# Kernel optimization log

Measured on AMD Instinct MI355X. Metric: run time of the kernel, lower is better.

## Reference

```python
import jax, jax.numpy as jnp
import numpy as np

D_MODEL = 512
N_HEADS = 8
D_FF = 2048

def _linear_params(key, d_in, d_out):
    kw, kb = jax.random.split(key)
    bound = 1.0 / np.sqrt(d_in)
    W = jax.random.uniform(kw, (d_in, d_out), minval=-bound, maxval=bound, dtype=jnp.float32)
    b = jax.random.uniform(kb, (d_out,), minval=-bound, maxval=bound, dtype=jnp.float32)
    return W, b

def setup_inputs() -> dict:
    key = jax.random.key(0)
    ks = jax.random.split(key, 7)
    x = jax.random.normal(ks[0], (4, 2048, D_MODEL), dtype=jnp.float32)
    Wq, bq = _linear_params(ks[1], D_MODEL, D_MODEL)
    Wk, bk = _linear_params(ks[2], D_MODEL, D_MODEL)
    Wv, bv = _linear_params(ks[3], D_MODEL, D_MODEL)
    W1, b1 = _linear_params(ks[4], D_MODEL, D_FF)
    W2, b2 = _linear_params(ks[5], D_FF, D_MODEL)
    g1 = jnp.ones((D_MODEL,), jnp.float32); be1 = jnp.zeros((D_MODEL,), jnp.float32)
    g2 = jnp.ones((D_MODEL,), jnp.float32); be2 = jnp.zeros((D_MODEL,), jnp.float32)
    return {"x": x, "Wq": Wq, "bq": bq, "Wk": Wk, "bk": bk, "Wv": Wv, "bv": bv,
            "W1": W1, "b1": b1, "W2": W2, "b2": b2,
            "g1": g1, "be1": be1, "g2": g2, "be2": be2}

def _layernorm(x, g, b, eps=1e-5):
    mu = jnp.mean(x, axis=-1, keepdims=True)
    var = jnp.mean(jnp.square(x - mu), axis=-1, keepdims=True)
    return (x - mu) * jax.lax.rsqrt(var + eps) * g + b

def reference(x, Wq, bq, Wk, bk, Wv, bv, W1, b1, W2, b2, g1, be1, g2, be2):
    B, S, D = x.shape
    H = N_HEADS
    Dh = D // H
    residual = x
    xn = _layernorm(x, g1, be1)
    # [B,S,D] -> [B,H,S,Dh]
    q = (xn @ Wq + bq).reshape(B, S, H, Dh).transpose(0, 2, 1, 3)
    k = (xn @ Wk + bk).reshape(B, S, H, Dh).transpose(0, 2, 1, 3)
    v = (xn @ Wv + bv).reshape(B, S, H, Dh).transpose(0, 2, 1, 3)
    # sigmoid pointwise attention, scaled by sqrt(d_model) (not head dim)
    scores = jnp.einsum('bhsd,bhtd->bhst', q, k) / jnp.sqrt(jnp.float32(D))
    attn = jax.nn.sigmoid(scores)
    out = jnp.einsum('bhst,bhtd->bhsd', attn, v)
    out = out.transpose(0, 2, 1, 3).reshape(B, S, D)
    x = residual + out  # dropout=0 (eval)
    residual = x
    xn = _layernorm(x, g2, be2)
    ffn = jax.nn.relu(xn @ W1 + b1) @ W2 + b2
    return residual + ffn
```

## Files before the change

kernel.cpp:

```cpp
#include <hip/hip_runtime.h>
#include <hip/hip_bf16.h>
#include <math.h>

#define D_MODEL 512
#define N_HEADS 8
#define D_HEAD 64
#define D_FF 2048
#define SEQ 2048
#define BATCH 4
#define NTOK (BATCH * SEQ)
#define QSCALE 0.04419417382415922f

typedef unsigned short ushort_t;
typedef __attribute__((ext_vector_type(8))) short short8;
typedef __attribute__((ext_vector_type(4))) float float4v;

static __device__ __forceinline__ ushort_t f2bf(float f) {
    union { float f; unsigned int i; } c; c.f = f;
    unsigned int i = c.i;
    unsigned int r = (i + 0x7FFFu + ((i >> 16) & 1u)) >> 16;
    return (ushort_t)r;
}

static __device__ __forceinline__ unsigned int pack2bf(float a, float b) {
    union { __hip_bfloat162 h; unsigned int u; } c;
    c.h = __float22bfloat162_rn(make_float2(a, b));
    return c.u;
}

static __device__ __forceinline__ float sigmoid_f(float x) {
    return __builtin_amdgcn_rcpf(1.0f + __expf(-x));
}

__global__ __launch_bounds__(256) void k_transpose_w(const float* __restrict__ W,
                                                     ushort_t* __restrict__ Wt,
                                                     int K, int N) {
    int id = blockIdx.x * 256 + threadIdx.x;
    if (id >= K * N) return;
    int k = id / N, n = id - k * N;
    Wt[(size_t)n * K + k] = f2bf(W[id]);
}

__global__ __launch_bounds__(256) void k_layernorm(const float* __restrict__ X,
                                                   const float* __restrict__ g,
                                                   const float* __restrict__ be,
                                                   ushort_t* __restrict__ Out) {
    int row  = blockIdx.x * 4 + (threadIdx.x >> 6);
    int lane = threadIdx.x & 63;
    const float* x = X + (size_t)row * D_MODEL + lane * 8;
    float4 v0 = ((const float4*)x)[0];
    float4 v1 = ((const float4*)x)[1];
    float vals[8] = {v0.x, v0.y, v0.z, v0.w, v1.x, v1.y, v1.z, v1.w};
    float s = 0.f, sq = 0.f;
#pragma unroll
    for (int j = 0; j < 8; j++) { s += vals[j]; sq += vals[j] * vals[j]; }
#pragma unroll
    for (int off = 32; off; off >>= 1) { s += __shfl_xor(s, off); sq += __shfl_xor(sq, off); }
    float mu  = s * (1.0f / D_MODEL);
    float var = sq * (1.0f / D_MODEL) - mu * mu;
    float inv = rsqrtf(var + 1e-5f);
    const float* gp  = g  + lane * 8;
    const float* bp  = be + lane * 8;
    float4 g0 = ((const float4*)gp)[0], g1v = ((const float4*)gp)[1];
    float4 b0 = ((const float4*)bp)[0], b1v = ((const float4*)bp)[1];
    float gs[8] = {g0.x, g0.y, g0.z, g0.w, g1v.x, g1v.y, g1v.z, g1v.w};
    float bs[8] = {b0.x, b0.y, b0.z, b0.w, b1v.x, b1v.y, b1v.z, b1v.w};
    ushort_t o[8];
#pragma unroll
    for (int j = 0; j < 8; j++) o[j] = f2bf((vals[j] - mu) * inv * gs[j] + bs[j]);
    ushort_t* op = Out + (size_t)row * D_MODEL + lane * 8;
    *(uint4*)op = *(uint4*)o;
}

__device__ __forceinline__ void gemm_core(const ushort_t* __restrict__ A,
                                          const ushort_t* __restrict__ Bt,
                                          int K, int m0, int n0,
                                          ushort_t (*As)[128][40], ushort_t (*Bs)[128][40],
                                          float4v acc[4][4]) {
    int t = threadIdx.x, w = t >> 6, l = t & 63, q = l >> 4, lm = l & 15;
    int mb = (w & 1) * 64, nb = (w >> 1) * 64;
    int srow = t >> 1, scol = (t & 1) * 16;
    const ushort_t* ag0 = A  + (size_t)(m0 + srow) * K + scol;
    const ushort_t* bg0 = Bt + (size_t)(n0 + srow) * K + scol;

    uint4 ar0 = *(const uint4*)(ag0),     ar1 = *(const uint4*)(ag0 + 8);
    uint4 br0 = *(const uint4*)(bg0),     br1 = *(const uint4*)(bg0 + 8);
    *(uint4*)&As[0][srow][scol] = ar0; *(uint4*)&As[0][srow][scol + 8] = ar1;
    *(uint4*)&Bs[0][srow][scol] = br0; *(uint4*)&Bs[0][srow][scol + 8] = br1;
    int T = K >> 5;
    ar0 = *(const uint4*)(ag0 + 32); ar1 = *(const uint4*)(ag0 + 40);
    br0 = *(const uint4*)(bg0 + 32); br1 = *(const uint4*)(bg0 + 40);
    __syncthreads();

    for (int kt = 0; kt < T; kt++) {
        int cur = kt & 1;
        short8 a[4], b[4];
#pragma unroll
        for (int i = 0; i < 4; i++) a[i] = *(const short8*)&As[cur][mb + 16 * i + lm][q * 8];
#pragma unroll
        for (int j = 0; j < 4; j++) b[j] = *(const short8*)&Bs[cur][nb + 16 * j + lm][q * 8];
#pragma unroll
        for (int i = 0; i < 4; i++)
#pragma unroll
            for (int j = 0; j < 4; j++)
                acc[i][j] = __builtin_amdgcn_mfma_f32_16x16x32_bf16(a[i], b[j], acc[i][j], 0, 0, 0);
        if (kt + 1 < T) {
            int nxt = 1 - cur;
            *(uint4*)&As[nxt][srow][scol] = ar0; *(uint4*)&As[nxt][srow][scol + 8] = ar1;
            *(uint4*)&Bs[nxt][srow][scol] = br0; *(uint4*)&Bs[nxt][srow][scol + 8] = br1;
            if (kt + 2 < T) {
                const ushort_t* ag = ag0 + (kt + 2) * 32;
                const ushort_t* bg = bg0 + (kt + 2) * 32;
                ar0 = *(const uint4*)(ag); ar1 = *(const uint4*)(ag + 8);
                br0 = *(const uint4*)(bg); br1 = *(const uint4*)(bg + 8);
            }
        }
        __syncthreads();
    }
}

__global__ __launch_bounds__(256) void k_gemm_qkv(const ushort_t* __restrict__ A,
                                                  const ushort_t* __restrict__ Bt,
                                                  const float* __restrict__ bq,
                                                  const float* __restrict__ bk,
                                                  const float* __restrict__ bv,
                                                  ushort_t* __restrict__ qb,
                                                  ushort_t* __restrict__ kb,
                                                  ushort_t* __restrict__ vt) {
    __shared__ ushort_t As[2][128][40];
    __shared__ ushort_t Bs[2][128][40];
    int m0 = blockIdx.x * 128, n0 = blockIdx.y * 128;
    float4v acc[4][4];
#pragma unroll
    for (int i = 0; i < 4; i++)
#pragma unroll
        for (int j = 0; j < 4; j++) acc[i][j] = (float4v){0.f, 0.f, 0.f, 0.f};
    gemm_core(A, Bt, D_MODEL, m0, n0, As, Bs, acc);

    int t = threadIdx.x, w = t >> 6, l = t & 63, q = l >> 4, lm = l & 15;
    int mb = (w & 1) * 64, nb = (w >> 1) * 64;
    int mat = n0 >> 9, c0 = n0 & 511;
    const float* bias = (mat == 0) ? bq : ((mat == 1) ? bk : bv);
#pragma unroll
    for (int j = 0; j < 4; j++) {
        int cl = c0 + nb + 16 * j + lm;
        int hh = cl >> 6, dh = cl & 63;
        float bvv = bias[cl];
#pragma unroll
        for (int i = 0; i < 4; i++) {
            int mr0 = m0 + mb + 16 * i + q * 4;
            int bb = mr0 >> 11, ss0 = mr0 & (SEQ - 1);
            if (mat == 2) {
                union { ushort_t s[4]; uint2 v; } pk;
#pragma unroll
                for (int r = 0; r < 4; r++) pk.s[r] = f2bf(acc[i][j][r] + bvv);
                *(uint2*)&vt[((size_t)(bb * N_HEADS + hh) * D_HEAD + dh) * SEQ + ss0] = pk.v;
            } else {
                ushort_t* dst = (mat == 0) ? qb : kb;
                float sc = (mat == 0) ? QSCALE : 1.0f;
#pragma unroll
                for (int r = 0; r < 4; r++)
                    dst[((size_t)(bb * N_HEADS + hh) * SEQ + ss0 + r) * D_HEAD + dh] =
                        f2bf((acc[i][j][r] + bvv) * sc);
            }
        }
    }
}

__global__ __launch_bounds__(256) void k_gemm_ffn1(const ushort_t* __restrict__ A,
                                                   const ushort_t* __restrict__ Bt,
                                                   const float* __restrict__ b1,
                                                   ushort_t* __restrict__ hb) {
    __shared__ ushort_t As[2][128][40];
    __shared__ ushort_t Bs[2][128][40];
    int m0 = blockIdx.x * 128, n0 = blockIdx.y * 128;
    float4v acc[4][4];
#pragma unroll
    for (int i = 0; i < 4; i++)
#pragma unroll
        for (int j = 0; j < 4; j++) acc[i][j] = (float4v){0.f, 0.f, 0.f, 0.f};
    gemm_core(A, Bt, D_MODEL, m0, n0, As, Bs, acc);

    int t = threadIdx.x, w = t >> 6, l = t & 63, q = l >> 4, lm = l & 15;
    int mb = (w & 1) * 64, nb = (w >> 1) * 64;
#pragma unroll
    for (int j = 0; j < 4; j++) {
        int cl = n0 + nb + 16 * j + lm;
        float bvv = b1[cl];
#pragma unroll
        for (int i = 0; i < 4; i++) {
            int mr0 = m0 + mb + 16 * i + q * 4;
#pragma unroll
            for (int r = 0; r < 4; r++)
                hb[(size_t)(mr0 + r) * D_FF + cl] = f2bf(fmaxf(acc[i][j][r] + bvv, 0.f));
        }
    }
}

__global__ __launch_bounds__(256) void k_gemm_ffn2(const ushort_t* __restrict__ A,
                                                   const ushort_t* __restrict__ Bt,
                                                   const float* __restrict__ b2,
                                                   const float* __restrict__ res,
                                                   float* __restrict__ out) {
    __shared__ ushort_t As[2][128][40];
    __shared__ ushort_t Bs[2][128][40];
    int m0 = blockIdx.x * 128, n0 = blockIdx.y * 128;
    float4v acc[4][4];
#pragma unroll
    for (int i = 0; i < 4; i++)
#pragma unroll
        for (int j = 0; j < 4; j++) acc[i][j] = (float4v){0.f, 0.f, 0.f, 0.f};
    gemm_core(A, Bt, D_FF, m0, n0, As, Bs, acc);

    int t = threadIdx.x, w = t >> 6, l = t & 63, q = l >> 4, lm = l & 15;
    int mb = (w & 1) * 64, nb = (w >> 1) * 64;
#pragma unroll
    for (int j = 0; j < 4; j++) {
        int cl = n0 + nb + 16 * j + lm;
        float bvv = b2[cl];
#pragma unroll
        for (int i = 0; i < 4; i++) {
            int mr0 = m0 + mb + 16 * i + q * 4;
#pragma unroll
            for (int r = 0; r < 4; r++) {
                size_t idx = (size_t)(mr0 + r) * D_MODEL + cl;
                out[idx] = acc[i][j][r] + bvv + res[idx];
            }
        }
    }
}

__global__ __launch_bounds__(256) void k_attention(const ushort_t* __restrict__ Q,
                                                   const ushort_t* __restrict__ Kb,
                                                   const ushort_t* __restrict__ Vt,
                                                   const float* __restrict__ X,
                                                   float* __restrict__ Y) {
    __shared__ ushort_t Ks[2][64][72];
    __shared__ ushort_t Vs[2][64][72];
    __shared__ ushort_t Ps[128][72];
    int bh = blockIdx.y;
    int b = bh >> 3, h = bh & 7;
    size_t base = (size_t)bh * SEQ * D_HEAD;
    int s0 = blockIdx.x * 128;
    int t = threadIdx.x, w = t >> 6, l = t & 63, q = l >> 4, lm = l & 15;
    int srow = t >> 2, sc = (t & 3) * 16;

    short8 qf[2][2];
#pragma unroll
    for (int nt = 0; nt < 2; nt++)
#pragma unroll
        for (int kc = 0; kc < 2; kc++) {
            const ushort_t* qg = Q + base + (size_t)(s0 + 32 * w + 16 * nt + lm) * D_HEAD + kc * 32 + q * 8;
            uint4 u = *(const uint4*)qg;
            qf[nt][kc] = *(const short8*)&u;
        }

    float4v o[2][4];
#pragma unroll
    for (int nt = 0; nt < 2; nt++)
#pragma unroll
        for (int dj = 0; dj < 4; dj++) o[nt][dj] = (float4v){0.f, 0.f, 0.f, 0.f};

    uint4 kr0, kr1, vr0, vr1;
    const ushort_t* kg0 = Kb + base + (size_t)srow * D_HEAD + sc;
    const ushort_t* vg0 = Vt + base + (size_t)srow * SEQ + sc;

    kr0 = *(const uint4*)(kg0); kr1 = *(const uint4*)(kg0 + 8);
    vr0 = *(const uint4*)(vg0); vr1 = *(const uint4*)(vg0 + 8);
    *(uint4*)&Ks[0][srow][sc] = kr0; *(uint4*)&Ks[0][srow][sc + 8] = kr1;
    *(uint4*)&Vs[0][srow][sc] = vr0; *(uint4*)&Vs[0][srow][sc + 8] = vr1;
    kr0 = *(const uint4*)(kg0 + 64 * D_HEAD); kr1 = *(const uint4*)(kg0 + 64 * D_HEAD + 8);
    vr0 = *(const uint4*)(vg0 + 64);          vr1 = *(const uint4*)(vg0 + 64 + 8);
    __syncthreads();

    for (int tt = 0; tt < SEQ / 64; tt++) {
        int cur = tt & 1;
        float4v st[4][2];
#pragma unroll
        for (int mt = 0; mt < 4; mt++)
#pragma unroll
            for (int nt = 0; nt < 2; nt++) st[mt][nt] = (float4v){0.f, 0.f, 0.f, 0.f};
#pragma unroll
        for (int kc = 0; kc < 2; kc++) {
            short8 a[4];
#pragma unroll
            for (int mt = 0; mt < 4; mt++) a[mt] = *(const short8*)&Ks[cur][16 * mt + lm][kc * 32 + q * 8];
#pragma unroll
            for (int mt = 0; mt < 4; mt++)
#pragma unroll
                for (int nt = 0; nt < 2; nt++)
                    st[mt][nt] = __builtin_amdgcn_mfma_f32_16x16x32_bf16(a[mt], qf[nt][kc], st[mt][nt], 0, 0, 0);
        }
#pragma unroll
        for (int mt = 0; mt < 4; mt++)
#pragma unroll
            for (int nt = 0; nt < 2; nt++) {
                float4v s4 = st[mt][nt];
                uint2 pk;
                pk.x = pack2bf(sigmoid_f(s4[0]), sigmoid_f(s4[1]));
                pk.y = pack2bf(sigmoid_f(s4[2]), sigmoid_f(s4[3]));
                *(uint2*)&Ps[32 * w + 16 * nt + lm][16 * mt + 4 * q] = pk;
            }
#pragma unroll
        for (int kc = 0; kc < 2; kc++) {
            short8 ap[2], bv[4];
#pragma unroll
            for (int nt = 0; nt < 2; nt++) ap[nt] = *(const short8*)&Ps[32 * w + 16 * nt + lm][kc * 32 + q * 8];
#pragma unroll
            for (int dj = 0; dj < 4; dj++) bv[dj] = *(const short8*)&Vs[cur][16 * dj + lm][kc * 32 + q * 8];
#pragma unroll
            for (int nt = 0; nt < 2; nt++)
#pragma unroll
                for (int dj = 0; dj < 4; dj++)
                    o[nt][dj] = __builtin_amdgcn_mfma_f32_16x16x32_bf16(ap[nt], bv[dj], o[nt][dj], 0, 0, 0);
        }
        if (tt + 1 < SEQ / 64) {
            int nxt = 1 - cur;
            *(uint4*)&Ks[nxt][srow][sc] = kr0; *(uint4*)&Ks[nxt][srow][sc + 8] = kr1;
            *(uint4*)&Vs[nxt][srow][sc] = vr0; *(uint4*)&Vs[nxt][srow][sc + 8] = vr1;
            if (tt + 2 < SEQ / 64) {
                const ushort_t* kg = kg0 + (size_t)(tt + 2) * 64 * D_HEAD;
                const ushort_t* vg = vg0 + (tt + 2) * 64;
                kr0 = *(const uint4*)(kg); kr1 = *(const uint4*)(kg + 8);
                vr0 = *(const uint4*)(vg); vr1 = *(const uint4*)(vg + 8);
            }
        }
        __syncthreads();
    }

#pragma unroll
    for (int nt = 0; nt < 2; nt++)
#pragma unroll
        for (int dj = 0; dj < 4; dj++) {
            int d = 16 * dj + lm;
#pragma unroll
            for (int r = 0; r < 4; r++) {
                int s = s0 + 32 * w + 16 * nt + q * 4 + r;
                size_t idx = ((size_t)(b * SEQ + s)) * D_MODEL + h * D_HEAD + d;
                Y[idx] = X[idx] + o[nt][dj][r];
            }
        }
}

extern "C" void kernel_launch(void* const* d_in, const int* in_sizes, int n_in,
                              void* d_out, int out_size, void* d_ws, size_t ws_size,
                              hipStream_t stream) {
    const float* x   = (const float*)d_in[0];
    const float* Wq  = (const float*)d_in[1];
    const float* bq  = (const float*)d_in[2];
    const float* Wk  = (const float*)d_in[3];
    const float* bk  = (const float*)d_in[4];
    const float* Wv  = (const float*)d_in[5];
    const float* bv  = (const float*)d_in[6];
    const float* W1  = (const float*)d_in[7];
    const float* b1  = (const float*)d_in[8];
    const float* W2  = (const float*)d_in[9];
    const float* b2  = (const float*)d_in[10];
    const float* g1  = (const float*)d_in[11];
    const float* be1 = (const float*)d_in[12];
    const float* g2  = (const float*)d_in[13];
    const float* be2 = (const float*)d_in[14];
    float* out = (float*)d_out;

    char* p = (char*)d_ws;
    ushort_t* xn    = (ushort_t*)p; p += (size_t)NTOK * D_MODEL * 2;
    ushort_t* yn    = (ushort_t*)p; p += (size_t)NTOK * D_MODEL * 2;
    float*    y     = (float*)p;    p += (size_t)NTOK * D_MODEL * 4;
    ushort_t* qb    = (ushort_t*)p; p += (size_t)NTOK * D_MODEL * 2;
    ushort_t* kb    = (ushort_t*)p; p += (size_t)NTOK * D_MODEL * 2;
    ushort_t* vt    = (ushort_t*)p; p += (size_t)NTOK * D_MODEL * 2;
    ushort_t* hb    = (ushort_t*)p; p += (size_t)NTOK * D_FF * 2;
    ushort_t* Wqkvt = (ushort_t*)p; p += (size_t)3 * D_MODEL * D_MODEL * 2;
    ushort_t* W1t   = (ushort_t*)p; p += (size_t)D_MODEL * D_FF * 2;
    ushort_t* W2t   = (ushort_t*)p; p += (size_t)D_FF * D_MODEL * 2;

    k_transpose_w<<<(D_MODEL * D_MODEL + 255) / 256, 256, 0, stream>>>(Wq, Wqkvt, D_MODEL, D_MODEL);
    k_transpose_w<<<(D_MODEL * D_MODEL + 255) / 256, 256, 0, stream>>>(Wk, Wqkvt + (size_t)D_MODEL * D_MODEL, D_MODEL, D_MODEL);
    k_transpose_w<<<(D_MODEL * D_MODEL + 255) / 256, 256, 0, stream>>>(Wv, Wqkvt + (size_t)2 * D_MODEL * D_MODEL, D_MODEL, D_MODEL);
    k_transpose_w<<<(D_MODEL * D_FF + 255) / 256, 256, 0, stream>>>(W1, W1t, D_MODEL, D_FF);
    k_transpose_w<<<(D_FF * D_MODEL + 255) / 256, 256, 0, stream>>>(W2, W2t, D_FF, D_MODEL);

    k_layernorm<<<NTOK / 4, 256, 0, stream>>>(x, g1, be1, xn);

    dim3 gq(NTOK / 128, (3 * D_MODEL) / 128);
    k_gemm_qkv<<<gq, 256, 0, stream>>>(xn, Wqkvt, bq, bk, bv, qb, kb, vt);

    dim3 ga(SEQ / 128, BATCH * N_HEADS);
    k_attention<<<ga, 256, 0, stream>>>(qb, kb, vt, x, y);

    k_layernorm<<<NTOK / 4, 256, 0, stream>>>(y, g2, be2, yn);

    dim3 g1d(NTOK / 128, D_FF / 128);
    k_gemm_ffn1<<<g1d, 256, 0, stream>>>(yn, W1t, b1, hb);
    dim3 g2d(NTOK / 128, D_MODEL / 128);
    k_gemm_ffn2<<<g2d, 256, 0, stream>>>(hb, W2t, b2, y, out);
}
```

Before: 275.0 us.

## Keep attention probabilities in registers, merge weight-prep kernels, vectorize output

The attention kernel now feeds the sigmoid probabilities straight from the score MFMA accumulators into a 16x16x16 bf16 MFMA as register operands. This removes the shared-memory P buffer and its write/read round trip, and computes the transposed output with V as the A operand. The five weight-transpose launches are merged into one kernel to cut launch overhead. The attention epilogue now does float4 residual loads and stores instead of scalar ones. The trade-off is using the smaller-K MFMA instruction, which means more MFMA issues for the same work.

Result: no change. 274.8 us (-0.1%).

```diff
diff --git a/kernel.cpp b/kernel.cpp
--- a/kernel.cpp
+++ b/kernel.cpp
@@ -13,6 +13,7 @@
 
 typedef unsigned short ushort_t;
 typedef __attribute__((ext_vector_type(8))) short short8;
+typedef __attribute__((ext_vector_type(4))) short short4v;
 typedef __attribute__((ext_vector_type(4))) float float4v;
 
 static __device__ __forceinline__ ushort_t f2bf(float f) {
@@ -32,13 +33,33 @@
     return __builtin_amdgcn_rcpf(1.0f + __expf(-x));
 }
 
-__global__ __launch_bounds__(256) void k_transpose_w(const float* __restrict__ W,
-                                                     ushort_t* __restrict__ Wt,
-                                                     int K, int N) {
+__global__ __launch_bounds__(256) void k_prep_weights(const float* __restrict__ Wq,
+                                                      const float* __restrict__ Wk,
+                                                      const float* __restrict__ Wv,
+                                                      const float* __restrict__ W1,
+                                                      const float* __restrict__ W2,
+                                                      ushort_t* __restrict__ Wqkvt,
+                                                      ushort_t* __restrict__ W1t,
+                                                      ushort_t* __restrict__ W2t) {
     int id = blockIdx.x * 256 + threadIdx.x;
-    if (id >= K * N) return;
-    int k = id / N, n = id - k * N;
-    Wt[(size_t)n * K + k] = f2bf(W[id]);
+    if (id < 3 * 262144) {
+        int m = id >> 18, r = id & 262143;
+        int k = r >> 9, n = r & 511;
+        const float* src = (m == 0) ? Wq : ((m == 1) ? Wk : Wv);
+        Wqkvt[((size_t)m * 512 + n) * 512 + k] = f2bf(src[r]);
+        return;
+    }
+    int id2 = id - 3 * 262144;
+    if (id2 < 1048576) {
+        int k = id2 >> 11, n = id2 & 2047;
+        W1t[(size_t)n * 512 + k] = f2bf(W1[id2]);
+        return;
+    }
+    int id3 = id2 - 1048576;
+    if (id3 < 1048576) {
+        int k = id3 >> 9, n = id3 & 511;
+        W2t[(size_t)n * 2048 + k] = f2bf(W2[id3]);
+    }
 }
 
 __global__ __launch_bounds__(256) void k_layernorm(const float* __restrict__ X,
@@ -237,7 +258,6 @@
                                                    float* __restrict__ Y) {
     __shared__ ushort_t Ks[2][64][72];
     __shared__ ushort_t Vs[2][64][72];
-    __shared__ ushort_t Ps[128][72];
     int bh = blockIdx.y;
     int b = bh >> 3, h = bh & 7;
     size_t base = (size_t)bh * SEQ * D_HEAD;
@@ -255,11 +275,11 @@
             qf[nt][kc] = *(const short8*)&u;
         }
 
-    float4v o[2][4];
-#pragma unroll
-    for (int nt = 0; nt < 2; nt++)
-#pragma unroll
-        for (int dj = 0; dj < 4; dj++) o[nt][dj] = (float4v){0.f, 0.f, 0.f, 0.f};
+    float4v o[4][2];
+#pragma unroll
+    for (int dj = 0; dj < 4; dj++)
+#pragma unroll
+        for (int nt = 0; nt < 2; nt++) o[dj][nt] = (float4v){0.f, 0.f, 0.f, 0.f};
 
     uint4 kr0, kr1, vr0, vr1;
     const ushort_t* kg0 = Kb + base + (size_t)srow * D_HEAD + sc;
@@ -291,28 +311,28 @@
                 for (int nt = 0; nt < 2; nt++)
                     st[mt][nt] = __builtin_amdgcn_mfma_f32_16x16x32_bf16(a[mt], qf[nt][kc], st[mt][nt], 0, 0, 0);
         }
+        short4v pf[4][2];
 #pragma unroll
         for (int mt = 0; mt < 4; mt++)
 #pragma unroll
             for (int nt = 0; nt < 2; nt++) {
                 float4v s4 = st[mt][nt];
-                uint2 pk;
-                pk.x = pack2bf(sigmoid_f(s4[0]), sigmoid_f(s4[1]));
-                pk.y = pack2bf(sigmoid_f(s4[2]), sigmoid_f(s4[3]));
-                *(uint2*)&Ps[32 * w + 16 * nt + lm][16 * mt + 4 * q] = pk;
+                union { unsigned int u[2]; short4v v; } pk;
+                pk.u[0] = pack2bf(sigmoid_f(s4[0]), sigmoid_f(s4[1]));
+                pk.u[1] = pack2bf(sigmoid_f(s4[2]), sigmoid_f(s4[3]));
+                pf[mt][nt] = pk.v;
             }
 #pragma unroll
-        for (int kc = 0; kc < 2; kc++) {
-            short8 ap[2], bv[4];
-#pragma unroll
-            for (int nt = 0; nt < 2; nt++) ap[nt] = *(const short8*)&Ps[32 * w + 16 * nt + lm][kc * 32 + q * 8];
-#pragma unroll
-            for (int dj = 0; dj < 4; dj++) bv[dj] = *(const short8*)&Vs[cur][16 * dj + lm][kc * 32 + q * 8];
-#pragma unroll
-            for (int nt = 0; nt < 2; nt++)
-#pragma unroll
-                for (int dj = 0; dj < 4; dj++)
-                    o[nt][dj] = __builtin_amdgcn_mfma_f32_16x16x32_bf16(ap[nt], bv[dj], o[nt][dj], 0, 0, 0);
+        for (int mt = 0; mt < 4; mt++) {
+            short4v vf[4];
+#pragma unroll
+            for (int dj = 0; dj < 4; dj++)
+                vf[dj] = *(const short4v*)&Vs[cur][16 * dj + lm][16 * mt + 4 * q];
+#pragma unroll
+            for (int dj = 0; dj < 4; dj++)
+#pragma unroll
+                for (int nt = 0; nt < 2; nt++)
+                    o[dj][nt] = __builtin_amdgcn_mfma_f32_16x16x16bf16_1k(vf[dj], pf[mt][nt], o[dj][nt], 0, 0, 0);
         }
         if (tt + 1 < SEQ / 64) {
             int nxt = 1 - cur;
@@ -329,17 +349,22 @@
     }
 
 #pragma unroll
-    for (int nt = 0; nt < 2; nt++)
+    for (int nt = 0; nt < 2; nt++) {
+        int s = s0 + 32 * w + 16 * nt + lm;
+        size_t rowoff = ((size_t)(b * SEQ + s)) * D_MODEL + h * D_HEAD;
+        const float* xp = X + rowoff;
+        float* yp = Y + rowoff;
 #pragma unroll
         for (int dj = 0; dj < 4; dj++) {
-            int d = 16 * dj + lm;
-#pragma unroll
-            for (int r = 0; r < 4; r++) {
-                int s = s0 + 32 * w + 16 * nt + q * 4 + r;
-                size_t idx = ((size_t)(b * SEQ + s)) * D_MODEL + h * D_HEAD + d;
-                Y[idx] = X[idx] + o[nt][dj][r];
-            }
-        }
+            int d0 = 16 * dj + 4 * q;
+            float4 xv = *(const float4*)(xp + d0);
+            float4v ov = o[dj][nt];
+            float4 r;
+            r.x = xv.x + ov[0]; r.y = xv.y + ov[1];
+            r.z = xv.z + ov[2]; r.w = xv.w + ov[3];
+            *(float4*)(yp + d0) = r;
+        }
+    }
 }
 
 extern "C" void kernel_launch(void* const* d_in, const int* in_sizes, int n_in,
@@ -374,11 +399,8 @@
     ushort_t* W1t   = (ushort_t*)p; p += (size_t)D_MODEL * D_FF * 2;
     ushort_t* W2t   = (ushort_t*)p; p += (size_t)D_FF * D_MODEL * 2;
 
-    k_transpose_w<<<(D_MODEL * D_MODEL + 255) / 256, 256, 0, stream>>>(Wq, Wqkvt, D_MODEL, D_MODEL);
-    k_transpose_w<<<(D_MODEL * D_MODEL + 255) / 256, 256, 0, stream>>>(Wk, Wqkvt + (size_t)D_MODEL * D_MODEL, D_MODEL, D_MODEL);
-    k_transpose_w<<<(D_MODEL * D_MODEL + 255) / 256, 256, 0, stream>>>(Wv, Wqkvt + (size_t)2 * D_MODEL * D_MODEL, D_MODEL, D_MODEL);
-    k_transpose_w<<<(D_MODEL * D_FF + 255) / 256, 256, 0, stream>>>(W1, W1t, D_MODEL, D_FF);
-    k_transpose_w<<<(D_FF * D_MODEL + 255) / 256, 256, 0, stream>>>(W2, W2t, D_FF, D_MODEL);
+    k_prep_weights<<<(3 * 262144 + 2 * 1048576 + 255) / 256, 256, 0, stream>>>(
+        Wq, Wk, Wv, W1, W2, Wqkvt, W1t, W2t);
 
     k_layernorm<<<NTOK / 4, 256, 0, stream>>>(x, g1, be1, xn);
 
```
